# Kernel optimization log

Hardware: AMD Instinct MI355X
Metric: run time of the kernel (lower is better)

## Reference

```python
import jax, jax.numpy as jnp
import numpy as np
from math import factorial, sqrt

L_MAX = 3
L_MAX_OUT = 3
NUM_SHELLS = 3
NUM_SH = (L_MAX + 1) ** 2  # 16 spherical-harmonic kernel components
SPLIT = [2 * l + 1 for l in range(L_MAX + 1)]  # [1,3,5,7]


def _su2_cg(j1, m1, j2, m2, j3, m3):
    """Clebsch-Gordan coefficient <j1 m1 j2 m2 | j3 m3> via the Racah formula."""
    if m3 != m1 + m2:
        return 0.0
    f = factorial
    vmin = max(-j1 + j2 + m3, -j1 + m1, 0)
    vmax = min(j2 + j3 + m1, j3 - j1 + j2, j3 + m3)
    c = sqrt((2 * j3 + 1) * f(j3 + j1 - j2) * f(j3 - j1 + j2) * f(j1 + j2 - j3) / f(j1 + j2 + j3 + 1)
             * f(j3 + m3) * f(j3 - m3) / (f(j1 - m1) * f(j1 + m1) * f(j2 - m2) * f(j2 + m2)))
    s = 0.0
    for v in range(vmin, vmax + 1):
        s += (-1.0) ** (v + j2 + m2) * f(j2 + j3 + m1 - v) * f(j1 - m1 + v) / (
            f(v) * f(j3 - j1 + j2 - v) * f(j3 + m3 - v) * f(v + j1 - j2 - m3))
    return c * s


def _real_to_complex(l):
    q = np.zeros((2 * l + 1, 2 * l + 1), dtype=np.complex128)
    for m in range(-l, 0):
        q[l + m, l + abs(m)] = 1 / sqrt(2)
        q[l + m, l - abs(m)] = -1j / sqrt(2)
    q[l, l] = 1.0
    for m in range(1, l + 1):
        q[l + m, l + abs(m)] = (-1) ** m / sqrt(2)
        q[l + m, l - abs(m)] = 1j * (-1) ** m / sqrt(2)
    return (-1j) ** l * q  # phase makes the real-basis CG purely real


def _real_cg(j, l, J):
    # CG coupling tensor in the real spherical-harmonic basis, shape (2j+1, 2l+1, 2J+1)
    C = np.zeros((2 * j + 1, 2 * l + 1, 2 * J + 1))
    for m1 in range(-j, j + 1):
        for m2 in range(-l, l + 1):
            for m3 in range(-J, J + 1):
                C[j + m1, l + m2, J + m3] = _su2_cg(j, m1, l, m2, J, m3)
    Cr = np.einsum('ij,kl,mn,ikm->jln', _real_to_complex(j), _real_to_complex(l),
                   np.conj(_real_to_complex(J)), C.astype(np.complex128))
    return np.real(Cr).astype(np.float32)  # imaginary part vanishes by phase choice


_CG = {(j, l, J): jnp.asarray(_real_cg(j, l, J))
       for j in range(1, L_MAX + 1) for l in range(1, L_MAX + 1)
       for J in range(abs(j - l), min(j + l, L_MAX_OUT) + 1)}


def setup_inputs() -> dict:
    key = jax.random.key(0)
    ks = jax.random.split(key, 6)
    b, n_src, n_tgt, p, C = 2, 4096, 2048, 32, 32
    return {
        'f0': jax.random.normal(ks[0], (b, n_src, 1, C), jnp.float32),
        'f1': jax.random.normal(ks[1], (b, n_src, 3, C), jnp.float32),
        'f2': jax.random.normal(ks[2], (b, n_src, 5, C), jnp.float32),
        'f3': jax.random.normal(ks[3], (b, n_src, 7, C), jnp.float32),
        'kernels': jax.random.normal(ks[4], (b, n_tgt, p, NUM_SH, NUM_SHELLS), jnp.float32),
        'patches_idx': jax.random.randint(ks[5], (b, n_tgt, p), 0, n_src, jnp.int32),
    }


def reference(f0, f1, f2, f3, kernels, patches_idx):
    feats = [f0, f1, f2, f3]
    b, n_src = f0.shape[0], f0.shape[1]
    ch_split = [(2 * l + 1) * feats[l].shape[-1] for l in range(L_MAX + 1)]
    # flatten each degree block and concatenate: (b, n_src, sum (2l+1)*C_l)
    signal = jnp.concatenate([f.reshape(b, n_src, -1) for f in feats], axis=-1)
    # gather per-target-point patches: (b, n_tgt, p, Ct)
    patches = jax.vmap(lambda s, i: s[i])(signal, patches_idx)
    n_tgt, p = patches_idx.shape[1], patches_idx.shape[2]
    S = kernels.shape[-1]
    K = kernels.reshape(b, n_tgt, p, -1)  # (b, n_tgt, p, NUM_SH*S)
    # kernel-weighted patch contraction
    y = jnp.einsum('bvpy,bvpc->bvyc', K, patches)  # (b, n_tgt, NUM_SH*S, Ct)
    y_parts = jnp.split(y, list(np.cumsum(ch_split)[:-1]), axis=-1)
    sh_cuts = list(np.cumsum(SPLIT)[:-1])
    out = {J: [] for J in range(L_MAX_OUT + 1)}
    cg_terms = []
    for l in range(L_MAX + 1):
        Cl = feats[l].shape[-1]
        yi = y_parts[l].reshape(b, n_tgt, NUM_SH, S, 2 * l + 1, Cl)
        yi = jnp.transpose(yi, (0, 1, 2, 4, 3, 5)).reshape(b, n_tgt, NUM_SH, 2 * l + 1, S * Cl)
        yjs = jnp.split(yi, sh_cuts, axis=2)
        for j in range(L_MAX + 1):
            yij = yjs[j]  # (b, n_tgt, 2j+1, 2l+1, S*Cl)
            if l == 0:
                out[j].append(yij[:, :, :, 0, :])
            elif j == 0:
                out[l].append(yij[:, :, 0, :, :])
            else:
                cg_terms.append((j, l, yij))
    # sparse Clebsch-Gordan tensor-product decomposition
    for j, l, yij in cg_terms:
        for J in range(abs(j - l), min(j + l, L_MAX_OUT) + 1):
            out[J].append(jnp.einsum('xyz,bvxyc->bvzc', _CG[(j, l, J)], yij))
    return tuple(jnp.concatenate(out[J], axis=-1) for J in range(L_MAX_OUT + 1))
```

## Files before the change

### kernel.cpp

```cpp
#include <hip/hip_runtime.h>
#include <hip/hip_bf16.h>

#define NTGT 2048
#define NSRC 4096
#define NPATCH 32
#define NY 48
#define NCG 3436
#define NTERMS 34
#define PITCH 132
#define NSLOTS 1024
#define DESC_OFF 16384

using short8 = __attribute__((ext_vector_type(8))) short;
using f32x4  = __attribute__((ext_vector_type(4))) float;

__constant__ int T_j[NTERMS]    = {0,1,2,3, 1,0,1,2,1,2,3,2,3, 2,0,1,2,3,1,2,3,1,2,3, 3,0,2,3,1,2,3,1,2,3};
__constant__ int T_l[NTERMS]    = {0,1,2,3, 0,1,1,1,2,2,2,3,3, 0,2,1,1,1,2,2,2,3,3,3, 0,3,1,1,2,2,2,3,3,3};
__constant__ int T_Jv[NTERMS]   = {0,0,0,0, 1,1,1,1,1,1,1,1,1, 2,2,2,2,2,2,2,2,2,2,2, 3,3,3,3,3,3,3,3,3,3};
__constant__ int T_cgoff[NTERMS]= {0,1,10,35, 84,93,102,129,174,219,294,399,504,
                                   651,676,701,746,821,926,1001,1126,1301,1406,1581,
                                   1826,1875,1924,2029,2176,2281,2456,2701,2848,3093};
__constant__ int T_col[NTERMS]  = {0,1,2,3, 0,1,2,3,4,5,6,7,8, 0,1,2,3,4,5,6,7,8,9,10, 0,1,2,3,4,5,6,7,8,9};
__constant__ int OUT_BASE[4] = {0, 1572864, 12189696, 33816576};
__constant__ int OUT_W[4]    = {384, 864, 1056, 960};
__constant__ int NJW_C[4]    = {384, 2592, 5280, 6720};
__constant__ int LI_L[16]  = {0,1,1,1,2,2,2,2,2,3,3,3,3,3,3,3};
__constant__ int LI_ML[16] = {0,0,1,2,0,1,2,3,4,0,1,2,3,4,5,6};
__constant__ int LI_WQ[16] = {1,3,3,3,5,5,5,5,5,7,7,7,7,7,7,7};
__constant__ int SEQ_TERM[NTERMS] = {3,12,23,33, 10,20,30, 11,22,32, 2,9,19,29,
                                     17,27, 21,31, 7,16,26, 8,18,28, 1,6,15,
                                     24,13,4,0, 25,14,5};
__constant__ int SEQ_BASE[NTERMS] = {0,6,24,54, 96,114,144, 186,204,234, 276,282,300,330,
                                     372,402, 444,474, 516,534,564, 606,624,654, 696,702,720,
                                     750,792,822,840, 846,888,918};

__device__ double factd(int n) { double r = 1.0; for (int i = 2; i <= n; ++i) r *= i; return r; }

__device__ double su2_cg(int j1, int m1, int j2, int m2, int j3, int m3) {
  if (m3 != m1 + m2) return 0.0;
  int vmin = max(max(-j1 + j2 + m3, -j1 + m1), 0);
  int vmax = min(min(j2 + j3 + m1, j3 - j1 + j2), j3 + m3);
  double cc = sqrt((2.0*j3 + 1.0) * factd(j3 + j1 - j2) * factd(j3 - j1 + j2) * factd(j1 + j2 - j3)
                   / factd(j1 + j2 + j3 + 1)
                   * factd(j3 + m3) * factd(j3 - m3)
                   / (factd(j1 - m1) * factd(j1 + m1) * factd(j2 - m2) * factd(j2 + m2)));
  double s = 0.0;
  for (int v = vmin; v <= vmax; ++v) {
    double sgn = ((v + j2 + m2) & 1) ? -1.0 : 1.0;
    s += sgn * factd(j2 + j3 + m1 - v) * factd(j1 - m1 + v)
         / (factd(v) * factd(j3 - j1 + j2 - v) * factd(j3 + m3 - v) * factd(v + j1 - j2 - m3));
  }
  return cc * s;
}

struct C2 { double re, im; };

__device__ C2 qent(int l, int r, int c) {
  double re = 0.0, im = 0.0;
  const double is2 = 0.70710678118654752440;
  int m = r - l;
  if (m < 0) {
    if (c == l - m) re = is2;
    else if (c == l + m) im = -is2;
  } else if (m == 0) {
    if (c == l) re = 1.0;
  } else {
    double sgn = (m & 1) ? -1.0 : 1.0;
    if (c == l + m) re = sgn * is2;
    else if (c == l - m) im = sgn * is2;
  }
  const double pr[4] = {1.0, 0.0, -1.0, 0.0};
  const double pi[4] = {0.0, -1.0, 0.0, 1.0};
  double a = pr[l & 3], bb = pi[l & 3];
  C2 o; o.re = re * a - im * bb; o.im = re * bb + im * a; return o;
}

__global__ void cg_init_kernel(float* __restrict__ cg) {
  __shared__ double su2_tab[49];
  const int t = blockIdx.x;
  const int j = T_j[t], l = T_l[t], J = T_Jv[t], off = T_cgoff[t];
  const int nj = 2*j + 1, nl = 2*l + 1, nJ = 2*J + 1;
  const bool triv = (l == 0 || j == 0);
  if (!triv) {
    for (int ik = threadIdx.x; ik < nj * nl; ik += blockDim.x) {
      int i = ik / nl, k = ik - (ik / nl) * nl;
      int m = (i - j) + (k - l) + J;
      su2_tab[ik] = (m >= 0 && m <= 2*J) ? su2_cg(j, i - j, l, k - l, J, m - J) : 0.0;
    }
  }
  __syncthreads();
  const int n = nj * nl * nJ;
  for (int e = threadIdx.x; e < n; e += blockDim.x) {
    int a = e / (nl * nJ);
    int r = e - a * nl * nJ;
    int bb = r / nJ;
    int cc = r - bb * nJ;
    float v;
    if (j == 0 && l == 0)      v = 1.0f;
    else if (l == 0)           v = (a == cc) ? 1.0f : 0.0f;
    else if (j == 0)           v = (bb == cc) ? 1.0f : 0.0f;
    else {
      double acc = 0.0;
      for (int i = 0; i < nj; ++i) {
        for (int k = 0; k < nl; ++k) {
          int m = (i - j) + (k - l) + J;
          if (m < 0 || m > 2*J) continue;
          double s2 = su2_tab[i * nl + k];
          if (s2 == 0.0) continue;
          C2 qa = qent(j, i, a), qb = qent(l, k, bb), qc = qent(J, m, cc);
          double r1 = qa.re * qb.re - qa.im * qb.im;
          double i1 = qa.re * qb.im + qa.im * qb.re;
          acc += (r1 * qc.re + i1 * qc.im) * s2;
        }
      }
      v = (float)acc;
    }
    cg[off + e] = v;
  }
}

__global__ void desc_init_kernel(uint2* __restrict__ desc) {
  const int t = blockIdx.x;
  const int term = SEQ_TERM[t];
  const int j = T_j[term], l = T_l[term], J = T_Jv[term];
  const int n = (2*J + 1) * 6;
  const int base = SEQ_BASE[t];
  for (int i = threadIdx.x; i < n; i += blockDim.x) {
    const int z = i / 6, r = i - (i / 6) * 6;
    const int s = r >> 1, ch4 = r & 1;
    uint2 d;
    d.x = (unsigned)(OUT_BASE[J] + T_col[term] * 96 + s * 32 + ch4 * 4 + z * OUT_W[J]);
    d.y = (unsigned)((j*j*3 + s) * PITCH + l*l*8 + ch4*4)
        | ((unsigned)(T_cgoff[term] + z) << 12)
        | ((unsigned)j << 24) | ((unsigned)l << 26) | ((unsigned)J << 28);
    desc[base + i] = d;
  }
  if (t == NTERMS - 1) {
    for (int s2 = 936 + threadIdx.x; s2 < NSLOTS; s2 += blockDim.x)
      desc[s2] = make_uint2(0u, 0x70000000u);
  }
}

__device__ __forceinline__ unsigned bfb(float x) {
  union { __hip_bfloat16 h; unsigned short u; } c;
  c.h = __float2bfloat16(x);
  return (unsigned)c.u;
}

__global__ __launch_bounds__(512, 6) void sh_conv_kernel(
    const float* __restrict__ f0, const float* __restrict__ f1,
    const float* __restrict__ f2, const float* __restrict__ f3,
    const float* __restrict__ kern, const int* __restrict__ pidx,
    const float* __restrict__ cg, const uint2* __restrict__ desc,
    float* __restrict__ out) {
  __shared__ float y_lds[NY * PITCH];
  __shared__ float cg_lds[NCG];
  const int tid = threadIdx.x;
  const int lane = tid & 63, wid = tid >> 6;
  const int g = lane >> 4, lr = lane & 15;
  const int xcd  = blockIdx.x & 7;
  const int slot = blockIdx.x >> 3;
  const int bv   = ((slot >> 2) << 3) | xcd;
  const int cb   = slot & 3;
  const int b    = bv >> 11;

  for (int i = tid; i < NCG; i += 512) cg_lds[i] = cg[i];

  const int ipv = pidx[(size_t)bv * NPATCH + (lane & 31)];
  int idx8[8];
  #pragma unroll
  for (int r = 0; r < 8; ++r) idx8[r] = __shfl(ipv, g * 8 + r);

  const float* kB = kern + (size_t)bv * (NPATCH * NY);
  short8 afr[3];
  #pragma unroll
  for (int m = 0; m < 3; ++m) {
    short8 af;
    #pragma unroll
    for (int r = 0; r < 8; ++r)
      af[r] = (short)bfb(kB[(g*8 + r) * NY + m*16 + lr]);
    afr[m] = af;
  }

  const int li  = wid * 2 + (lr >> 3);
  const int chl = lr & 7;
  const int l_  = LI_L[li], mlv = LI_ML[li], wq = LI_WQ[li];
  const float* fp = (l_ == 0) ? f0 : (l_ == 1) ? f1 : (l_ == 2) ? f2 : f3;
  const float* base = fp + ((size_t)b * NSRC) * (wq * 32) + mlv * 32 + cb * 8 + chl;
  short8 bfr;
  #pragma unroll
  for (int r = 0; r < 8; ++r)
    bfr[r] = (short)bfb(base[(size_t)(idx8[r] * wq) << 5]);

  f32x4 acc0 = {0.f,0.f,0.f,0.f}, acc1 = {0.f,0.f,0.f,0.f}, acc2 = {0.f,0.f,0.f,0.f};
  acc0 = __builtin_amdgcn_mfma_f32_16x16x32_bf16(afr[0], bfr, acc0, 0, 0, 0);
  acc1 = __builtin_amdgcn_mfma_f32_16x16x32_bf16(afr[1], bfr, acc1, 0, 0, 0);
  acc2 = __builtin_amdgcn_mfma_f32_16x16x32_bf16(afr[2], bfr, acc2, 0, 0, 0);

  #pragma unroll
  for (int q = 0; q < 4; ++q) {
    y_lds[(0*16 + g*4 + q) * PITCH + wid*16 + lr] = acc0[q];
    y_lds[(1*16 + g*4 + q) * PITCH + wid*16 + lr] = acc1[q];
    y_lds[(2*16 + g*4 + q) * PITCH + wid*16 + lr] = acc2[q];
  }

  __syncthreads();

  #pragma unroll 1
  for (int rnd = 0; rnd < 2; ++rnd) {
    const uint2 d = desc[rnd * 512 + tid];
    const unsigned w1 = d.y;
    const int J = (w1 >> 28) & 7;
    if (J > 3) continue;
    const int j = (w1 >> 24) & 3, l = (w1 >> 26) & 3;
    const int nj = 2*j + 1, nl = 2*l + 1, nJ = 2*J + 1;
    const float* yb  = y_lds + (w1 & 0xFFF);
    const float* cgp = cg_lds + ((w1 >> 12) & 0xFFF);
    float a0 = 0.f, a1 = 0.f, a2 = 0.f, a3 = 0.f;
    int cgi = 0;
    #pragma unroll 1
    for (int mj = 0; mj < nj; ++mj) {
      const float* yr = yb + mj * 3 * PITCH;
      #pragma unroll 1
      for (int ml = 0; ml < nl; ++ml) {
        const float4 yq = *(const float4*)(yr + ml * 8);
        const float c = cgp[cgi]; cgi += nJ;
        a0 = fmaf(c, yq.x, a0); a1 = fmaf(c, yq.y, a1);
        a2 = fmaf(c, yq.z, a2); a3 = fmaf(c, yq.w, a3);
      }
    }
    const size_t addr = (size_t)d.x + (size_t)bv * NJW_C[J] + cb * 8;
    float4 o; o.x = a0; o.y = a1; o.z = a2; o.w = a3;
    *(float4*)&out[addr] = o;
  }
}

extern "C" void kernel_launch(void* const* d_in, const int* in_sizes, int n_in,
                              void* d_out, int out_size, void* d_ws, size_t ws_size,
                              hipStream_t stream) {
  const float* f0   = (const float*)d_in[0];
  const float* f1   = (const float*)d_in[1];
  const float* f2   = (const float*)d_in[2];
  const float* f3   = (const float*)d_in[3];
  const float* kern = (const float*)d_in[4];
  const int*   pidx = (const int*)d_in[5];
  float* out  = (float*)d_out;
  float* cg   = (float*)d_ws;
  uint2* desc = (uint2*)((char*)d_ws + DESC_OFF);

  hipLaunchKernelGGL(cg_init_kernel, dim3(NTERMS), dim3(256), 0, stream, cg);
  hipLaunchKernelGGL(desc_init_kernel, dim3(NTERMS), dim3(64), 0, stream, desc);
  hipLaunchKernelGGL(sh_conv_kernel, dim3(4 * 2 * NTGT), dim3(512), 0, stream,
                     f0, f1, f2, f3, kern, pidx, cg, desc, out);
}
```

Before: 199.9 us.

## Group CG work into wave-uniform shape classes with compile-time unrolled contraction

Reorganises the CG descriptor table so each wave processes rounds of a single (j,l) shape class, assigned through a static wave-to-round schedule. The contraction then dispatches to fully unrolled templated loops instead of runtime-bounded nested loops. The CG table is re-laid out as contiguous 16-byte-aligned rows per output component, and trivial copy terms get their own class. This removes loop overhead and wave divergence from mixed shapes, at the cost of a hand-built static schedule, an extra memset launch and a slightly larger LDS table.

```diff
diff --git a/kernel.cpp b/kernel.cpp
--- a/kernel.cpp
+++ b/kernel.cpp
@@ -5,21 +5,18 @@
 #define NSRC 4096
 #define NPATCH 32
 #define NY 48
-#define NCG 3436
-#define NTERMS 34
 #define PITCH 132
-#define NSLOTS 1024
+#define NCG2 3524
+#define NSLOTS 1280
 #define DESC_OFF 16384
 
 using short8 = __attribute__((ext_vector_type(8))) short;
 using f32x4  = __attribute__((ext_vector_type(4))) float;
 
+#define NTERMS 34
 __constant__ int T_j[NTERMS]    = {0,1,2,3, 1,0,1,2,1,2,3,2,3, 2,0,1,2,3,1,2,3,1,2,3, 3,0,2,3,1,2,3,1,2,3};
 __constant__ int T_l[NTERMS]    = {0,1,2,3, 0,1,1,1,2,2,2,3,3, 0,2,1,1,1,2,2,2,3,3,3, 0,3,1,1,2,2,2,3,3,3};
 __constant__ int T_Jv[NTERMS]   = {0,0,0,0, 1,1,1,1,1,1,1,1,1, 2,2,2,2,2,2,2,2,2,2,2, 3,3,3,3,3,3,3,3,3,3};
-__constant__ int T_cgoff[NTERMS]= {0,1,10,35, 84,93,102,129,174,219,294,399,504,
-                                   651,676,701,746,821,926,1001,1126,1301,1406,1581,
-                                   1826,1875,1924,2029,2176,2281,2456,2701,2848,3093};
 __constant__ int T_col[NTERMS]  = {0,1,2,3, 0,1,2,3,4,5,6,7,8, 0,1,2,3,4,5,6,7,8,9,10, 0,1,2,3,4,5,6,7,8,9};
 __constant__ int OUT_BASE[4] = {0, 1572864, 12189696, 33816576};
 __constant__ int OUT_W[4]    = {384, 864, 1056, 960};
@@ -27,12 +24,15 @@
 __constant__ int LI_L[16]  = {0,1,1,1,2,2,2,2,2,3,3,3,3,3,3,3};
 __constant__ int LI_ML[16] = {0,0,1,2,0,1,2,3,4,0,1,2,3,4,5,6};
 __constant__ int LI_WQ[16] = {1,3,3,3,5,5,5,5,5,7,7,7,7,7,7,7};
-__constant__ int SEQ_TERM[NTERMS] = {3,12,23,33, 10,20,30, 11,22,32, 2,9,19,29,
-                                     17,27, 21,31, 7,16,26, 8,18,28, 1,6,15,
-                                     24,13,4,0, 25,14,5};
-__constant__ int SEQ_BASE[NTERMS] = {0,6,24,54, 96,114,144, 186,204,234, 276,282,300,330,
-                                     372,402, 444,474, 516,534,564, 606,624,654, 696,702,720,
-                                     750,792,822,840, 846,888,918};
+__constant__ int TERM_SLOT[NTERMS] = {1088,1024,384,0, 1094,1184,1030,896,768,390,256,128,6,
+                                      1112,1202,1048,914,640,786,408,274,512,146,24,
+                                      1142,1232,944,670,816,438,304,542,176,54};
+__constant__ int CG2OFF4[NTERMS] = {0,0,3,10, 0,0,23,32,44,56,77,104,131,
+                                    0,0,170,185,205,235,255,290,335,365,410,
+                                    0,0,475,503,545,573,622,685,727,790};
+__constant__ int RND_CLASS[20] = {0,0,1,1,2,2,3,3,4,4,5,5,6,6,7,7,8,9,9,9};
+__constant__ signed char WAVE_RNDS[8][3] = {
+  {0,17,-1},{1,16,-1},{2,8,-1},{3,9,18},{4,10,19},{5,11,-1},{6,14,13},{7,15,12}};
 
 __device__ double factd(int n) { double r = 1.0; for (int i = 2; i <= n; ++i) r *= i; return r; }
 
@@ -75,69 +75,59 @@
   C2 o; o.re = re * a - im * bb; o.im = re * bb + im * a; return o;
 }
 
-__global__ void cg_init_kernel(float* __restrict__ cg) {
+__global__ void cg_init_kernel(float* __restrict__ cg2) {
   __shared__ double su2_tab[49];
   const int t = blockIdx.x;
-  const int j = T_j[t], l = T_l[t], J = T_Jv[t], off = T_cgoff[t];
+  const int j = T_j[t], l = T_l[t], J = T_Jv[t];
+  if (j == 0 || l == 0) return;
   const int nj = 2*j + 1, nl = 2*l + 1, nJ = 2*J + 1;
-  const bool triv = (l == 0 || j == 0);
-  if (!triv) {
-    for (int ik = threadIdx.x; ik < nj * nl; ik += blockDim.x) {
-      int i = ik / nl, k = ik - (ik / nl) * nl;
-      int m = (i - j) + (k - l) + J;
-      su2_tab[ik] = (m >= 0 && m <= 2*J) ? su2_cg(j, i - j, l, k - l, J, m - J) : 0.0;
+  const int njnl = nj * nl, stride4 = (njnl + 3) >> 2;
+  for (int ik = threadIdx.x; ik < njnl; ik += blockDim.x) {
+    int i = ik / nl, k = ik - (ik / nl) * nl;
+    int m = (i - j) + (k - l) + J;
+    su2_tab[ik] = (m >= 0 && m <= 2*J) ? su2_cg(j, i - j, l, k - l, J, m - J) : 0.0;
+  }
+  __syncthreads();
+  const int n = nJ * njnl;
+  for (int e = threadIdx.x; e < n; e += blockDim.x) {
+    const int z = e / njnl, rr = e - (e / njnl) * njnl;
+    const int mj = rr / nl, ml = rr - (rr / nl) * nl;
+    double acc = 0.0;
+    for (int i = 0; i < nj; ++i) {
+      for (int k = 0; k < nl; ++k) {
+        int m = (i - j) + (k - l) + J;
+        if (m < 0 || m > 2*J) continue;
+        double s2 = su2_tab[i * nl + k];
+        if (s2 == 0.0) continue;
+        C2 qa = qent(j, i, mj), qb = qent(l, k, ml), qc = qent(J, m, z);
+        double r1 = qa.re * qb.re - qa.im * qb.im;
+        double i1 = qa.re * qb.im + qa.im * qb.re;
+        acc += (r1 * qc.re + i1 * qc.im) * s2;
+      }
     }
-  }
-  __syncthreads();
-  const int n = nj * nl * nJ;
-  for (int e = threadIdx.x; e < n; e += blockDim.x) {
-    int a = e / (nl * nJ);
-    int r = e - a * nl * nJ;
-    int bb = r / nJ;
-    int cc = r - bb * nJ;
-    float v;
-    if (j == 0 && l == 0)      v = 1.0f;
-    else if (l == 0)           v = (a == cc) ? 1.0f : 0.0f;
-    else if (j == 0)           v = (bb == cc) ? 1.0f : 0.0f;
-    else {
-      double acc = 0.0;
-      for (int i = 0; i < nj; ++i) {
-        for (int k = 0; k < nl; ++k) {
-          int m = (i - j) + (k - l) + J;
-          if (m < 0 || m > 2*J) continue;
-          double s2 = su2_tab[i * nl + k];
-          if (s2 == 0.0) continue;
-          C2 qa = qent(j, i, a), qb = qent(l, k, bb), qc = qent(J, m, cc);
-          double r1 = qa.re * qb.re - qa.im * qb.im;
-          double i1 = qa.re * qb.im + qa.im * qb.re;
-          acc += (r1 * qc.re + i1 * qc.im) * s2;
-        }
-      }
-      v = (float)acc;
-    }
-    cg[off + e] = v;
+    cg2[(CG2OFF4[t] + z * stride4) * 4 + rr] = (float)acc;
   }
 }
 
 __global__ void desc_init_kernel(uint2* __restrict__ desc) {
   const int t = blockIdx.x;
-  const int term = SEQ_TERM[t];
-  const int j = T_j[term], l = T_l[term], J = T_Jv[term];
+  const int j = T_j[t], l = T_l[t], J = T_Jv[t];
   const int n = (2*J + 1) * 6;
-  const int base = SEQ_BASE[t];
+  const int slot0 = TERM_SLOT[t];
+  const bool cp = (j == 0 || l == 0);
+  const int nl = 2*l + 1, njnl = (2*j + 1) * nl;
+  const int stride4 = (njnl + 3) >> 2;
   for (int i = threadIdx.x; i < n; i += blockDim.x) {
     const int z = i / 6, r = i - (i / 6) * 6;
     const int s = r >> 1, ch4 = r & 1;
-    uint2 d;
-    d.x = (unsigned)(OUT_BASE[J] + T_col[term] * 96 + s * 32 + ch4 * 4 + z * OUT_W[J]);
-    d.y = (unsigned)((j*j*3 + s) * PITCH + l*l*8 + ch4*4)
-        | ((unsigned)(T_cgoff[term] + z) << 12)
-        | ((unsigned)j << 24) | ((unsigned)l << 26) | ((unsigned)J << 28);
-    desc[base + i] = d;
-  }
-  if (t == NTERMS - 1) {
-    for (int s2 = 936 + threadIdx.x; s2 < NSLOTS; s2 += blockDim.x)
-      desc[s2] = make_uint2(0u, 0x70000000u);
+    const unsigned ob = (unsigned)(OUT_BASE[J] + T_col[t] * 96 + s * 32 + ch4 * 4 + z * OUT_W[J]);
+    int ybase;
+    if (!cp)         ybase = (j*j*3 + s) * PITCH + l*l*8 + ch4*4;
+    else if (l == 0) ybase = ((j*j + z)*3 + s) * PITCH + ch4*4;
+    else             ybase = s * PITCH + (l*l + z)*8 + ch4*4;
+    const unsigned cgb4 = (unsigned)(CG2OFF4[t] + z * stride4);
+    desc[slot0 + i] = make_uint2(ob,
+        (unsigned)(ybase >> 2) | (cgb4 << 11) | ((unsigned)J << 21) | 0x80000000u);
   }
 }
 
@@ -147,14 +137,30 @@
   return (unsigned)c.u;
 }
 
+template<int JT, int LT>
+__device__ __forceinline__ float4 pairc(const float4* __restrict__ yb4,
+                                        const float* __restrict__ cgp) {
+  constexpr int nl = 2*LT + 1, njnl = (2*JT + 1) * nl;
+  float a0 = 0.f, a1 = 0.f, a2 = 0.f, a3 = 0.f;
+  #pragma unroll
+  for (int e = 0; e < njnl; ++e) {
+    const int mj = e / nl, ml = e - (e / nl) * nl;
+    const float4 yq = yb4[mj * 99 + ml * 2];
+    const float c = cgp[e];
+    a0 = fmaf(c, yq.x, a0); a1 = fmaf(c, yq.y, a1);
+    a2 = fmaf(c, yq.z, a2); a3 = fmaf(c, yq.w, a3);
+  }
+  float4 o; o.x = a0; o.y = a1; o.z = a2; o.w = a3; return o;
+}
+
 __global__ __launch_bounds__(512, 6) void sh_conv_kernel(
     const float* __restrict__ f0, const float* __restrict__ f1,
     const float* __restrict__ f2, const float* __restrict__ f3,
     const float* __restrict__ kern, const int* __restrict__ pidx,
-    const float* __restrict__ cg, const uint2* __restrict__ desc,
+    const float* __restrict__ cg2, const uint2* __restrict__ desc,
     float* __restrict__ out) {
   __shared__ float y_lds[NY * PITCH];
-  __shared__ float cg_lds[NCG];
+  __shared__ float cg_lds[NCG2];
   const int tid = threadIdx.x;
   const int lane = tid & 63, wid = tid >> 6;
   const int g = lane >> 4, lr = lane & 15;
@@ -164,7 +170,7 @@
   const int cb   = slot & 3;
   const int b    = bv >> 11;
 
-  for (int i = tid; i < NCG; i += 512) cg_lds[i] = cg[i];
+  for (int i = tid; i < NCG2; i += 512) cg_lds[i] = cg2[i];
 
   const int ipv = pidx[(size_t)bv * NPATCH + (lane & 31)];
   int idx8[8];
@@ -206,32 +212,32 @@
 
   __syncthreads();
 
+  const int widu = __builtin_amdgcn_readfirstlane(wid);
+  const float4* yall = (const float4*)y_lds;
   #pragma unroll 1
-  for (int rnd = 0; rnd < 2; ++rnd) {
-    const uint2 d = desc[rnd * 512 + tid];
+  for (int ri = 0; ri < 3; ++ri) {
+    const int rnd = WAVE_RNDS[widu][ri];
+    if (rnd < 0) break;
+    const uint2 d = desc[(rnd << 6) | lane];
     const unsigned w1 = d.y;
-    const int J = (w1 >> 28) & 7;
-    if (J > 3) continue;
-    const int j = (w1 >> 24) & 3, l = (w1 >> 26) & 3;
-    const int nj = 2*j + 1, nl = 2*l + 1, nJ = 2*J + 1;
-    const float* yb  = y_lds + (w1 & 0xFFF);
-    const float* cgp = cg_lds + ((w1 >> 12) & 0xFFF);
-    float a0 = 0.f, a1 = 0.f, a2 = 0.f, a3 = 0.f;
-    int cgi = 0;
-    #pragma unroll 1
-    for (int mj = 0; mj < nj; ++mj) {
-      const float* yr = yb + mj * 3 * PITCH;
-      #pragma unroll 1
-      for (int ml = 0; ml < nl; ++ml) {
-        const float4 yq = *(const float4*)(yr + ml * 8);
-        const float c = cgp[cgi]; cgi += nJ;
-        a0 = fmaf(c, yq.x, a0); a1 = fmaf(c, yq.y, a1);
-        a2 = fmaf(c, yq.z, a2); a3 = fmaf(c, yq.w, a3);
-      }
+    const float4* yb4 = yall + (w1 & 0x7FF);
+    const float*  cgp = cg_lds + (((w1 >> 11) & 0x3FF) << 2);
+    const int J = (w1 >> 21) & 3;
+    float4 o;
+    switch (RND_CLASS[rnd]) {
+      case 0: o = pairc<3,3>(yb4, cgp); break;
+      case 1: o = pairc<2,3>(yb4, cgp); break;
+      case 2: o = pairc<3,2>(yb4, cgp); break;
+      case 3: o = pairc<2,2>(yb4, cgp); break;
+      case 4: o = pairc<1,3>(yb4, cgp); break;
+      case 5: o = pairc<3,1>(yb4, cgp); break;
+      case 6: o = pairc<1,2>(yb4, cgp); break;
+      case 7: o = pairc<2,1>(yb4, cgp); break;
+      case 8: o = pairc<1,1>(yb4, cgp); break;
+      default: o = yb4[0]; break;
     }
-    const size_t addr = (size_t)d.x + (size_t)bv * NJW_C[J] + cb * 8;
-    float4 o; o.x = a0; o.y = a1; o.z = a2; o.w = a3;
-    *(float4*)&out[addr] = o;
+    if (w1 >> 31)
+      *(float4*)&out[(size_t)d.x + (size_t)bv * NJW_C[J] + cb * 8] = o;
   }
 }
 
@@ -245,11 +251,12 @@
   const float* kern = (const float*)d_in[4];
   const int*   pidx = (const int*)d_in[5];
   float* out  = (float*)d_out;
-  float* cg   = (float*)d_ws;
+  float* cg2  = (float*)d_ws;
   uint2* desc = (uint2*)((char*)d_ws + DESC_OFF);
 
-  hipLaunchKernelGGL(cg_init_kernel, dim3(NTERMS), dim3(256), 0, stream, cg);
+  hipMemsetAsync(desc, 0, NSLOTS * sizeof(uint2), stream);
+  hipLaunchKernelGGL(cg_init_kernel, dim3(NTERMS), dim3(256), 0, stream, cg2);
   hipLaunchKernelGGL(desc_init_kernel, dim3(NTERMS), dim3(64), 0, stream, desc);
   hipLaunchKernelGGL(sh_conv_kernel, dim3(4 * 2 * NTGT), dim3(512), 0, stream,
-                     f0, f1, f2, f3, kern, pidx, cg, desc, out);
-}
+                     f0, f1, f2, f3, kern, pidx, cg2, desc, out);
+}
```

After: 213.5 us. +6.8%, slower.
